# Kernel optimization log

Hardware: AMD Instinct MI355X
Metric: run time of the kernel (lower is better)

## Reference

```python
import jax, jax.numpy as jnp
import numpy as np


def setup_inputs() -> dict:
    key = jax.random.key(0)
    ks = jax.random.split(key, 6)
    B, I, H, O = 4096, 2048, 2048, 2048
    return {
        "x": jax.random.normal(ks[0], (B, I), dtype=jnp.float32),
        "hidden": jax.random.normal(ks[1], (B, H), dtype=jnp.float32),
        "W_ih": jax.random.normal(ks[2], (H, I + H), dtype=jnp.float32) * (1.0 / np.sqrt(I + H)),
        "b_ih": jax.random.normal(ks[3], (H,), dtype=jnp.float32) * 0.01,
        "W_ho": jax.random.normal(ks[4], (O, H), dtype=jnp.float32) * (1.0 / np.sqrt(H)),
        "b_ho": jax.random.normal(ks[5], (O,), dtype=jnp.float32) * 0.01,
    }


def reference(x, hidden, W_ih, b_ih, W_ho, b_ho):
    # Fused RNN cell:
    #   combined   = [x, hidden]                      [B, I+H]
    #   new_hidden = tanh(combined @ W_ih^T + b_ih)   [B, H]
    #   output     = new_hidden @ W_ho^T + b_ho       [B, O]
    combined = jnp.concatenate([x, hidden], axis=-1)
    new_hidden = jnp.tanh(jnp.einsum('bk,hk->bh', combined, W_ih) + b_ih)
    output = jnp.einsum('bh,oh->bo', new_hidden, W_ho) + b_ho
    return output, new_hidden
```

## Files before the change

### kernel.cpp

```cpp
#include <hip/hip_runtime.h>
#include <hip/hip_bf16.h>

typedef unsigned short u16;
typedef __attribute__((ext_vector_type(8))) __bf16 bf16x8;
typedef __attribute__((ext_vector_type(4))) float f32x4;

__device__ __forceinline__ u16 f2bf(float f) {
    union { float f; unsigned u; } v; v.f = f;
    unsigned u = v.u;
    unsigned r = (u + 0x7FFFu + ((u >> 16) & 1u)) >> 16;
    return (u16)r;
}

__global__ void cvt_f32_bf16(const float4* __restrict__ src,
                             ushort4* __restrict__ dst, int n4) {
    int i = blockIdx.x * blockDim.x + threadIdx.x;
    if (i < n4) {
        float4 a = src[i];
        ushort4 o;
        o.x = f2bf(a.x); o.y = f2bf(a.y); o.z = f2bf(a.z); o.w = f2bf(a.w);
        dst[i] = o;
    }
}

#define BM 128
#define BN 128
#define BK 32

template<int MODE>
__global__ __launch_bounds__(256, 2)
void gemm_bt(const u16* __restrict__ A0, const u16* __restrict__ A1,
             const u16* __restrict__ Bm, const float* __restrict__ bias,
             float* __restrict__ Cf, u16* __restrict__ Cbf,
             int M, int N, int K)
{
    __shared__ u16 Alds[BM * BK];
    __shared__ u16 Blds[BN * BK];

    const int tid  = threadIdx.x;
    const int wave = tid >> 6;
    const int lane = tid & 63;
    const int nTiles = N / BN;
    const int mB = (int)blockIdx.x / nTiles;
    const int nB = (int)blockIdx.x % nTiles;
    const int m0 = mB * BM;
    const int n0 = nB * BN;

    const int wr = wave >> 1;
    const int wc = wave & 1;
    const int fr = lane & 15;
    const int fq = lane >> 4;

    f32x4 acc[4][4];
    #pragma unroll
    for (int i = 0; i < 4; ++i)
        #pragma unroll
        for (int j = 0; j < 4; ++j)
            acc[i][j] = f32x4{0.f, 0.f, 0.f, 0.f};

    const int lda   = (MODE == 0) ? 2048 : K;
    const int arow  = lane >> 2;
    const int acolc = (lane & 3) * 8;

    for (int k0 = 0; k0 < K; k0 += BK) {
        const u16* Asrc;
        int kc;
        if (MODE == 0) { Asrc = (k0 < 2048) ? A0 : A1; kc = k0 & 2047; }
        else           { Asrc = A0;                    kc = k0;        }

        #pragma unroll
        for (int j = 0; j < 2; ++j) {
            int row = wave * 32 + j * 16 + arow;
            const u16* g = Asrc + (size_t)(m0 + row) * lda + kc + acolc;
            __builtin_amdgcn_global_load_lds(
                (const __attribute__((address_space(1))) unsigned int*)g,
                (__attribute__((address_space(3))) unsigned int*)&Alds[(wave * 32 + j * 16) * BK],
                16, 0, 0);
        }
        #pragma unroll
        for (int j = 0; j < 2; ++j) {
            int row = wave * 32 + j * 16 + arow;
            const u16* g = Bm + (size_t)(n0 + row) * K + k0 + acolc;
            __builtin_amdgcn_global_load_lds(
                (const __attribute__((address_space(1))) unsigned int*)g,
                (__attribute__((address_space(3))) unsigned int*)&Blds[(wave * 32 + j * 16) * BK],
                16, 0, 0);
        }
        __syncthreads();

        bf16x8 af[4], bfr[4];
        #pragma unroll
        for (int i = 0; i < 4; ++i)
            af[i] = *reinterpret_cast<const bf16x8*>(
                &Alds[(wr * 64 + i * 16 + fr) * BK + fq * 8]);
        #pragma unroll
        for (int j = 0; j < 4; ++j)
            bfr[j] = *reinterpret_cast<const bf16x8*>(
                &Blds[(wc * 64 + j * 16 + fr) * BK + fq * 8]);

        #pragma unroll
        for (int i = 0; i < 4; ++i)
            #pragma unroll
            for (int j = 0; j < 4; ++j)
                acc[i][j] = __builtin_amdgcn_mfma_f32_16x16x32_bf16(
                    af[i], bfr[j], acc[i][j], 0, 0, 0);

        __syncthreads();
    }

    #pragma unroll
    for (int i = 0; i < 4; ++i) {
        #pragma unroll
        for (int j = 0; j < 4; ++j) {
            int col = n0 + wc * 64 + j * 16 + fr;
            float bv = bias[col];
            #pragma unroll
            for (int r = 0; r < 4; ++r) {
                int row = m0 + wr * 64 + i * 16 + fq * 4 + r;
                float v = acc[i][j][r] + bv;
                if constexpr (MODE == 0) {
                    v = tanhf(v);
                    Cf[(size_t)row * N + col]  = v;
                    Cbf[(size_t)row * N + col] = f2bf(v);
                } else {
                    Cf[(size_t)row * N + col] = v;
                }
            }
        }
    }
}

extern "C" void kernel_launch(void* const* d_in, const int* in_sizes, int n_in,
                              void* d_out, int out_size, void* d_ws, size_t ws_size,
                              hipStream_t stream) {
    const float* x   = (const float*)d_in[0];
    const float* hid = (const float*)d_in[1];
    const float* Wih = (const float*)d_in[2];
    const float* bih = (const float*)d_in[3];
    const float* Who = (const float*)d_in[4];
    const float* bho = (const float*)d_in[5];
    float* out = (float*)d_out;

    const int B = 4096, I = 2048, H = 2048, O = 2048;

    u16* x_bf   = (u16*)d_ws;
    u16* h_bf   = x_bf   + (size_t)B * I;
    u16* wih_bf = h_bf   + (size_t)B * H;
    u16* who_bf = wih_bf + (size_t)H * (I + H);
    u16* nh_bf  = who_bf + (size_t)O * H;

    auto cvt = [&](const float* s, u16* d, size_t n) {
        int n4 = (int)(n / 4);
        cvt_f32_bf16<<<dim3((n4 + 255) / 256), dim3(256), 0, stream>>>(
            (const float4*)s, (ushort4*)d, n4);
    };
    cvt(x,   x_bf,   (size_t)B * I);
    cvt(hid, h_bf,   (size_t)B * H);
    cvt(Wih, wih_bf, (size_t)H * (I + H));
    cvt(Who, who_bf, (size_t)O * H);

    float* out_y  = out;
    float* out_nh = out + (size_t)B * O;

    gemm_bt<0><<<dim3((B / 128) * (H / 128)), dim3(256), 0, stream>>>(
        x_bf, h_bf, wih_bf, bih, out_nh, nh_bf, B, H, I + H);

    gemm_bt<1><<<dim3((B / 128) * (O / 128)), dim3(256), 0, stream>>>(
        nh_bf, nh_bf, who_bf, bho, out_y, nullptr, B, O, H);
}
```

Baseline: 322.9 us.

## Triple-buffer GEMM with larger 256x128 tiles, swizzled LDS, and fused conversion

```diff
diff --git a/kernel.cpp b/kernel.cpp
--- a/kernel.cpp
+++ b/kernel.cpp
@@ -5,51 +5,65 @@
 typedef __attribute__((ext_vector_type(8))) __bf16 bf16x8;
 typedef __attribute__((ext_vector_type(4))) float f32x4;
 
+#define AS1 __attribute__((address_space(1)))
+#define AS3 __attribute__((address_space(3)))
+
 __device__ __forceinline__ u16 f2bf(float f) {
     union { float f; unsigned u; } v; v.f = f;
     unsigned u = v.u;
-    unsigned r = (u + 0x7FFFu + ((u >> 16) & 1u)) >> 16;
-    return (u16)r;
-}
-
-__global__ void cvt_f32_bf16(const float4* __restrict__ src,
-                             ushort4* __restrict__ dst, int n4) {
-    int i = blockIdx.x * blockDim.x + threadIdx.x;
-    if (i < n4) {
-        float4 a = src[i];
-        ushort4 o;
-        o.x = f2bf(a.x); o.y = f2bf(a.y); o.z = f2bf(a.z); o.w = f2bf(a.w);
-        dst[i] = o;
+    return (u16)((u + 0x7FFFu + ((u >> 16) & 1u)) >> 16);
+}
+
+__global__ void cvt4(const float4* __restrict__ a, const float4* __restrict__ b,
+                     const float4* __restrict__ c, const float4* __restrict__ d,
+                     ushort4* __restrict__ oa, ushort4* __restrict__ ob,
+                     ushort4* __restrict__ oc, ushort4* __restrict__ od,
+                     int na, int nb, int nc, int nd) {
+    const int total = na + nb + nc + nd;
+    for (int i = blockIdx.x * blockDim.x + threadIdx.x; i < total;
+         i += gridDim.x * blockDim.x) {
+        const float4* s; ushort4* o; int j = i;
+        if (j < na) { s = a; o = oa; }
+        else {
+            j -= na;
+            if (j < nb) { s = b; o = ob; }
+            else {
+                j -= nb;
+                if (j < nc) { s = c; o = oc; }
+                else        { j -= nc; s = d; o = od; }
+            }
+        }
+        float4 v = s[j];
+        ushort4 u;
+        u.x = f2bf(v.x); u.y = f2bf(v.y); u.z = f2bf(v.z); u.w = f2bf(v.w);
+        o[j] = u;
     }
 }
 
-#define BM 128
-#define BN 128
-#define BK 32
-
 template<int MODE>
-__global__ __launch_bounds__(256, 2)
+__global__ __launch_bounds__(512, 2)
 void gemm_bt(const u16* __restrict__ A0, const u16* __restrict__ A1,
              const u16* __restrict__ Bm, const float* __restrict__ bias,
              float* __restrict__ Cf, u16* __restrict__ Cbf,
              int M, int N, int K)
 {
-    __shared__ u16 Alds[BM * BK];
-    __shared__ u16 Blds[BN * BK];
-
+    extern __shared__ u16 lds[];
     const int tid  = threadIdx.x;
     const int wave = tid >> 6;
     const int lane = tid & 63;
-    const int nTiles = N / BN;
-    const int mB = (int)blockIdx.x / nTiles;
-    const int nB = (int)blockIdx.x % nTiles;
-    const int m0 = mB * BM;
-    const int n0 = nB * BN;
-
-    const int wr = wave >> 1;
-    const int wc = wave & 1;
-    const int fr = lane & 15;
-    const int fq = lane >> 4;
+
+    const int nN  = N >> 7;
+    const int nwg = (M >> 8) * nN;
+    const int id  = ((int)blockIdx.x % 8) * (nwg >> 3) + (int)blockIdx.x / 8;
+    const int m0  = (id / nN) << 8;
+    const int n0  = (id % nN) << 7;
+
+    const int fr = lane & 15, fq = lane >> 4;
+    const int wr = wave >> 1, wc = wave & 1;
+
+    const int srow   = tid >> 3;
+    const int schunk = (tid & 7) ^ (srow & 7);
+    const int ldsW   = wave << 9;
 
     f32x4 acc[4][4];
     #pragma unroll
@@ -58,65 +72,81 @@
         for (int j = 0; j < 4; ++j)
             acc[i][j] = f32x4{0.f, 0.f, 0.f, 0.f};
 
-    const int lda   = (MODE == 0) ? 2048 : K;
-    const int arow  = lane >> 2;
-    const int acolc = (lane & 3) * 8;
-
-    for (int k0 = 0; k0 < K; k0 += BK) {
-        const u16* Asrc;
-        int kc;
-        if (MODE == 0) { Asrc = (k0 < 2048) ? A0 : A1; kc = k0 & 2047; }
-        else           { Asrc = A0;                    kc = k0;        }
-
-        #pragma unroll
-        for (int j = 0; j < 2; ++j) {
-            int row = wave * 32 + j * 16 + arow;
-            const u16* g = Asrc + (size_t)(m0 + row) * lda + kc + acolc;
-            __builtin_amdgcn_global_load_lds(
-                (const __attribute__((address_space(1))) unsigned int*)g,
-                (__attribute__((address_space(3))) unsigned int*)&Alds[(wave * 32 + j * 16) * BK],
-                16, 0, 0);
-        }
-        #pragma unroll
-        for (int j = 0; j < 2; ++j) {
-            int row = wave * 32 + j * 16 + arow;
-            const u16* g = Bm + (size_t)(n0 + row) * K + k0 + acolc;
-            __builtin_amdgcn_global_load_lds(
-                (const __attribute__((address_space(1))) unsigned int*)g,
-                (__attribute__((address_space(3))) unsigned int*)&Blds[(wave * 32 + j * 16) * BK],
-                16, 0, 0);
-        }
-        __syncthreads();
-
-        bf16x8 af[4], bfr[4];
-        #pragma unroll
-        for (int i = 0; i < 4; ++i)
-            af[i] = *reinterpret_cast<const bf16x8*>(
-                &Alds[(wr * 64 + i * 16 + fr) * BK + fq * 8]);
-        #pragma unroll
-        for (int j = 0; j < 4; ++j)
-            bfr[j] = *reinterpret_cast<const bf16x8*>(
-                &Blds[(wc * 64 + j * 16 + fr) * BK + fq * 8]);
-
+    const int lda = (MODE == 0) ? 2048 : K;
+
+    auto stage = [&](int t) {
+        const int k0  = t << 6;
+        const int buf = (t % 3) * 24576;
+        const u16* As; int kc;
+        if constexpr (MODE == 0) { As = (k0 < 2048) ? A0 : A1; kc = k0 & 2047; }
+        else                     { As = A0;                    kc = k0;        }
+        #pragma unroll
+        for (int r = 0; r < 4; ++r) {
+            const u16* g = As + (size_t)(m0 + (r << 6) + srow) * lda + kc + (schunk << 3);
+            __builtin_amdgcn_global_load_lds((const AS1 unsigned int*)g,
+                (AS3 unsigned int*)&lds[buf + (r << 12) + ldsW], 16, 0, 0);
+        }
+        #pragma unroll
+        for (int r = 0; r < 2; ++r) {
+            const u16* g = Bm + (size_t)(n0 + (r << 6) + srow) * K + k0 + (schunk << 3);
+            __builtin_amdgcn_global_load_lds((const AS1 unsigned int*)g,
+                (AS3 unsigned int*)&lds[buf + 16384 + (r << 12) + ldsW], 16, 0, 0);
+        }
+    };
+
+    const int ax0 = ((fq)     ^ (fr & 7)) << 3;
+    const int ax1 = ((4 + fq) ^ (fr & 7)) << 3;
+    const int aoff = ((wr << 6) + fr) << 6;
+    const int boff = ((wc << 6) + fr) << 6;
+
+    const int nt = K >> 6;
+
+    stage(0); stage(1);
+    asm volatile("s_waitcnt vmcnt(6)" ::: "memory");
+    __builtin_amdgcn_s_barrier();
+
+    for (int t = 0; t < nt; ++t) {
+        const int buf = (t % 3) * 24576;
+        if (t + 2 < nt) stage(t + 2);
+
+        bf16x8 a0[4], a1[4], b0[4], b1[4];
+        #pragma unroll
+        for (int i = 0; i < 4; ++i) {
+            a0[i] = *(const bf16x8*)&lds[buf + aoff + (i << 10) + ax0];
+            a1[i] = *(const bf16x8*)&lds[buf + aoff + (i << 10) + ax1];
+        }
+        #pragma unroll
+        for (int j = 0; j < 4; ++j) {
+            b0[j] = *(const bf16x8*)&lds[buf + 16384 + boff + (j << 10) + ax0];
+            b1[j] = *(const bf16x8*)&lds[buf + 16384 + boff + (j << 10) + ax1];
+        }
+
+        __builtin_amdgcn_s_setprio(1);
         #pragma unroll
         for (int i = 0; i < 4; ++i)
             #pragma unroll
-            for (int j = 0; j < 4; ++j)
-                acc[i][j] = __builtin_amdgcn_mfma_f32_16x16x32_bf16(
-                    af[i], bfr[j], acc[i][j], 0, 0, 0);
-
-        __syncthreads();
+            for (int j = 0; j < 4; ++j) {
+                acc[i][j] = __builtin_amdgcn_mfma_f32_16x16x32_bf16(a0[i], b0[j], acc[i][j], 0, 0, 0);
+                acc[i][j] = __builtin_amdgcn_mfma_f32_16x16x32_bf16(a1[i], b1[j], acc[i][j], 0, 0, 0);
+            }
+        __builtin_amdgcn_s_setprio(0);
+
+        if (t + 1 < nt) {
+            if (t + 2 < nt) asm volatile("s_waitcnt vmcnt(6)" ::: "memory");
+            else            asm volatile("s_waitcnt vmcnt(0)" ::: "memory");
+            __builtin_amdgcn_s_barrier();
+        }
     }
 
     #pragma unroll
-    for (int i = 0; i < 4; ++i) {
-        #pragma unroll
-        for (int j = 0; j < 4; ++j) {
-            int col = n0 + wc * 64 + j * 16 + fr;
-            float bv = bias[col];
+    for (int j = 0; j < 4; ++j) {
+        const int col = n0 + (wc << 6) + (j << 4) + fr;
+        const float bv = bias[col];
+        #pragma unroll
+        for (int i = 0; i < 4; ++i) {
             #pragma unroll
             for (int r = 0; r < 4; ++r) {
-                int row = m0 + wr * 64 + i * 16 + fq * 4 + r;
+                const int row = m0 + (wr << 6) + (i << 4) + (fq << 2) + r;
                 float v = acc[i][j][r] + bv;
                 if constexpr (MODE == 0) {
                     v = tanhf(v);
@@ -149,22 +179,25 @@
     u16* who_bf = wih_bf + (size_t)H * (I + H);
     u16* nh_bf  = who_bf + (size_t)O * H;
 
-    auto cvt = [&](const float* s, u16* d, size_t n) {
-        int n4 = (int)(n / 4);
-        cvt_f32_bf16<<<dim3((n4 + 255) / 256), dim3(256), 0, stream>>>(
-            (const float4*)s, (ushort4*)d, n4);
-    };
-    cvt(x,   x_bf,   (size_t)B * I);
-    cvt(hid, h_bf,   (size_t)B * H);
-    cvt(Wih, wih_bf, (size_t)H * (I + H));
-    cvt(Who, who_bf, (size_t)O * H);
+    const int na = (B * I) / 4, nb = (B * H) / 4,
+              nc = (H * (I + H)) / 4, nd = (O * H) / 4;
+    cvt4<<<dim3(2048), dim3(256), 0, stream>>>(
+        (const float4*)x, (const float4*)hid, (const float4*)Wih, (const float4*)Who,
+        (ushort4*)x_bf, (ushort4*)h_bf, (ushort4*)wih_bf, (ushort4*)who_bf,
+        na, nb, nc, nd);
 
     float* out_y  = out;
     float* out_nh = out + (size_t)B * O;
 
-    gemm_bt<0><<<dim3((B / 128) * (H / 128)), dim3(256), 0, stream>>>(
+    const size_t shmem = 3 * 24576 * sizeof(u16);
+    hipFuncSetAttribute(reinterpret_cast<const void*>(&gemm_bt<0>),
+                        hipFuncAttributeMaxDynamicSharedMemorySize, (int)shmem);
+    hipFuncSetAttribute(reinterpret_cast<const void*>(&gemm_bt<1>),
+                        hipFuncAttributeMaxDynamicSharedMemorySize, (int)shmem);
+
+    gemm_bt<0><<<dim3((B / 256) * (H / 128)), dim3(512), shmem, stream>>>(
         x_bf, h_bf, wih_bf, bih, out_nh, nh_bf, B, H, I + H);
 
-    gemm_bt<1><<<dim3((B / 128) * (O / 128)), dim3(256), 0, stream>>>(
+    gemm_bt<1><<<dim3((B / 256) * (O / 128)), dim3(512), shmem, stream>>>(
         nh_bf, nh_bf, who_bf, bho, out_y, nullptr, B, O, H);
 }
```

Result: faster. 289.9 us (-10.2%).
